# Optimization experiments

Measured on AMD Instinct MI355X. Metric: run time of the kernel, lower is better.

## Reference

```python
import math
import jax, jax.numpy as jnp
import numpy as np

# ---- static config (EquiformerV2 defaults; num_layers reduced to 2) ----
L_MAX, M_MAX = 6, 2
NC = (L_MAX + 1) ** 2          # 49 SH coefficients
C = 128                        # sphere_channels
H = 128                        # attn_hidden_channels
HEADS, VPH = 8, 16             # num_heads, attn_value_channels
FFN = 512                      # ffn_hidden_channels
NB = 600                       # gaussian distance basis count
NLAYERS = 2
N, E, G = 2048, 12288, 16      # nodes, edges, graphs
AVG_DEG = 3.0                  # edge-degree rescale factor (_AVG_DEGREE)
CUTOFF = 5.0
DISC_LO, DISC_HI = -3.26267, 3.295396

_deg = np.array([l for l in range(L_MAX + 1) for m in range(-l, l + 1)])
_mv = np.array([m for l in range(L_MAX + 1) for m in range(-l, l + 1)])
RESTRICT = np.nonzero(np.abs(_mv) <= M_MAX)[0]       # 29 coeffs with |m|<=mmax
NR = len(RESTRICT)
DEG1H = np.eye(L_MAX + 1, dtype=np.float32)[_deg]    # [49,7]
DEG_CNT = DEG1H.sum(0)                               # 2l+1 per degree

_off = np.linspace(0.0, CUTOFF, NB).astype(np.float32)
_gcoef = np.float32(-0.5 / (2.0 * (_off[1] - _off[0])) ** 2)  # width scalar 2.0

def gaussian_smearing(d):
    return jnp.exp(_gcoef * (d[:, None] - jnp.asarray(_off)[None, :]) ** 2)

def real_sph_harm(vec):
    # real spherical harmonics Y_lm of edge directions, [E, 49], l-major, m=-l..l
    r = jnp.linalg.norm(vec, axis=-1, keepdims=True)
    u = vec / jnp.maximum(r, 1e-8)
    x, y, z = u[:, 0], u[:, 1], u[:, 2]
    ct = jnp.clip(z, -1.0, 1.0)
    st = jnp.sqrt(jnp.clip(1.0 - ct * ct, 1e-12, 1.0))
    phi = jnp.arctan2(y, x)
    P = {(0, 0): jnp.ones_like(ct)}
    for m in range(1, L_MAX + 1):
        P[(m, m)] = -(2 * m - 1) * st * P[(m - 1, m - 1)]
    for m in range(0, L_MAX):
        P[(m + 1, m)] = (2 * m + 1) * ct * P[(m, m)]
    for m in range(0, L_MAX + 1):
        for l in range(m + 2, L_MAX + 1):
            P[(l, m)] = ((2 * l - 1) * ct * P[(l - 1, m)] - (l + m - 1) * P[(l - 2, m)]) / (l - m)
    cols = []
    for l in range(L_MAX + 1):
        for m in range(-l, l + 1):
            am = abs(m)
            nrm = math.sqrt((2 * l + 1) / (4 * math.pi) * math.factorial(l - am) / math.factorial(l + am))
            if m == 0:
                cols.append(nrm * P[(l, 0)])
            elif m > 0:
                cols.append(math.sqrt(2.0) * nrm * P[(l, m)] * jnp.cos(m * phi))
            else:
                cols.append(math.sqrt(2.0) * nrm * P[(l, am)] * jnp.sin(am * phi))
    return jnp.stack(cols, axis=-1)

def rms_norm_sh(x, w, eps=1e-6):
    # per-degree RMS over (m, channels) with learned [7,C] scale
    d1h = jnp.asarray(DEG1H)
    ms = jnp.einsum('nkc,kl->nl', x * x, d1h) / (jnp.asarray(DEG_CNT) * C)
    inv = 1.0 / jnp.sqrt(ms + eps)                      # [N,7]
    wk = jnp.einsum('lc,kl->kc', w, d1h)                # [49,C]
    return x * (inv @ d1h.T)[:, :, None] * wk[None]

def so2_attention(x, dist, src, dst, w_s, w_t, rw1, rb1, rw2, avec, w_v, w_p):
    n = x.shape[0]
    ridx = jnp.asarray(RESTRICT)
    xr = x[:, ridx, :]                                   # [N,29,C] (|m|<=mmax)
    msg = xr[src] @ w_s + xr[dst] @ w_t                  # [E,29,H]
    rad = jax.nn.silu(dist @ rw1 + rb1) @ rw2            # [E,H] radial modulation
    msg = msg * rad[:, None, :]
    a = jax.nn.silu(msg[:, 0, :]).reshape(-1, HEADS, H // HEADS)
    logits = jnp.einsum('ehd,hd->eh', a, avec)           # [E,HEADS]
    mx = jax.ops.segment_max(logits, dst, num_segments=n)
    ex = jnp.exp(logits - mx[dst])
    den = jax.ops.segment_sum(ex, dst, num_segments=n)
    alpha = ex / jnp.maximum(den[dst], 1e-9)
    v = (msg @ w_v).reshape(-1, NR, HEADS, VPH) * alpha[:, None, :, None]
    agg = jax.ops.segment_sum(v.reshape(-1, NR, HEADS * VPH), dst, num_segments=n)
    out_r = agg @ w_p                                    # [N,29,C]
    return jnp.zeros_like(x).at[:, ridx, :].set(out_r)

def ffn_act(x, w1, w2):
    # separable S2 activation: silu on l=0 scalars, sigmoid-gated higher degrees
    h = jnp.einsum('nkc,cf->nkf', x, w1)
    s = h[:, 0, :]
    h = jnp.concatenate([jax.nn.silu(s)[:, None, :], h[:, 1:, :] * jax.nn.sigmoid(s)[:, None, :]], axis=1)
    return jnp.einsum('nkf,fc->nkc', h, w2)

def _forward(pos, edge_vec, edge_index, batch, embed_table, deg_w1, deg_b1, deg_w2, deg_b2, deg_w3, attn_norm_w, w_src, w_tgt, rad_w1, rad_b1, rad_w2, alpha_vec, w_val, w_proj, ffn_norm_w, ffn_w1, ffn_w2, final_norm_w, lat_w_src, lat_w_tgt, lat_rad_w1, lat_rad_b1, lat_rad_w2, lat_alpha, lat_w_val, lat_w_proj):
    src, dst = edge_index[0], edge_index[1]
    d = jnp.linalg.norm(edge_vec, axis=-1)
    dist = gaussian_smearing(d)                                  # [E,600]
    # scalar node init from discretized coordinates (3 embedding lookups summed)
    t = jnp.clip(jnp.round((pos - DISC_LO) / (DISC_HI - DISC_LO) * 128.0 - 0.5), 0, 127).astype(jnp.int32)
    emb = embed_table[t[:, 0]] + embed_table[t[:, 1]] + embed_table[t[:, 2]]
    x = jnp.zeros((N, NC, C), emb.dtype).at[:, 0, :].set(emb)
    # edge-degree embedding: radial weights x Y_lm(edge dir), scatter to targets
    rad = jax.nn.silu(jax.nn.silu(dist @ deg_w1 + deg_b1) @ deg_w2 + deg_b2) @ deg_w3
    rad = rad.reshape(E, L_MAX + 1, C)[:, jnp.asarray(_deg), :]  # [E,49,C]
    Y = real_sph_harm(edge_vec)                                  # [E,49]
    x = x + jax.ops.segment_sum(Y[:, :, None] * rad, dst, num_segments=N) / AVG_DEG
    for i in range(NLAYERS):
        h = rms_norm_sh(x, attn_norm_w[i])
        x = x + so2_attention(h, dist, src, dst, w_src[i], w_tgt[i], rad_w1[i], rad_b1[i], rad_w2[i], alpha_vec[i], w_val[i], w_proj[i])
        h = rms_norm_sh(x, ffn_norm_w[i])
        x = x + ffn_act(h, ffn_w1[i], ffn_w2[i])
    x = rms_norm_sh(x, final_norm_w)
    latent = so2_attention(x, dist, src, dst, lat_w_src, lat_w_tgt, lat_rad_w1, lat_rad_b1, lat_rad_w2, lat_alpha, lat_w_val, lat_w_proj)
    cnt = jax.ops.segment_sum(jnp.ones((N,), latent.dtype), batch, num_segments=G)
    pooled = jax.ops.segment_sum(latent, batch, num_segments=G) / jnp.maximum(cnt, 1.0)[:, None, None]
    return pooled.reshape(1, -1)

def setup_inputs() -> dict:
    key = jax.random.key(0)
    ks = iter(jax.random.split(key, 64))
    def nrm(shape, fan_in):
        return jax.random.normal(next(ks), shape, jnp.float32) * np.float32(1.0 / math.sqrt(fan_in))
    inp = {}
    inp['pos'] = jax.random.normal(next(ks), (N, 3), jnp.float32) * 1.5
    inp['edge_vec'] = jax.random.normal(next(ks), (E, 3), jnp.float32)
    inp['edge_index'] = jax.random.randint(next(ks), (2, E), 0, N)
    inp['batch'] = jnp.sort(jax.random.randint(next(ks), (N,), 0, G))
    inp['embed_table'] = nrm((128, C), C)
    inp['deg_w1'] = nrm((NB, C), NB); inp['deg_b1'] = jnp.zeros((C,), jnp.float32)
    inp['deg_w2'] = nrm((C, C), C); inp['deg_b2'] = jnp.zeros((C,), jnp.float32)
    inp['deg_w3'] = nrm((C, (L_MAX + 1) * C), C)
    inp['attn_norm_w'] = jnp.ones((NLAYERS, L_MAX + 1, C), jnp.float32)
    inp['w_src'] = nrm((NLAYERS, C, H), C)
    inp['w_tgt'] = nrm((NLAYERS, C, H), C)
    inp['rad_w1'] = nrm((NLAYERS, NB, H), NB); inp['rad_b1'] = jnp.zeros((NLAYERS, H), jnp.float32)
    inp['rad_w2'] = nrm((NLAYERS, H, H), H)
    inp['alpha_vec'] = nrm((NLAYERS, HEADS, H // HEADS), H // HEADS)
    inp['w_val'] = nrm((NLAYERS, H, HEADS * VPH), H)
    inp['w_proj'] = nrm((NLAYERS, HEADS * VPH, C), HEADS * VPH)
    inp['ffn_norm_w'] = jnp.ones((NLAYERS, L_MAX + 1, C), jnp.float32)
    inp['ffn_w1'] = nrm((NLAYERS, C, FFN), C)
    inp['ffn_w2'] = nrm((NLAYERS, FFN, C), FFN)
    inp['final_norm_w'] = jnp.ones((L_MAX + 1, C), jnp.float32)
    inp['lat_w_src'] = nrm((C, H), C); inp['lat_w_tgt'] = nrm((C, H), C)
    inp['lat_rad_w1'] = nrm((NB, H), NB); inp['lat_rad_b1'] = jnp.zeros((H,), jnp.float32)
    inp['lat_rad_w2'] = nrm((H, H), H)
    inp['lat_alpha'] = nrm((HEADS, H // HEADS), H // HEADS)
    inp['lat_w_val'] = nrm((H, HEADS * VPH), H)
    inp['lat_w_proj'] = nrm((HEADS * VPH, C), HEADS * VPH)
    return inp

def reference(pos, edge_vec, edge_index, batch, embed_table, deg_w1, deg_b1, deg_w2, deg_b2, deg_w3, attn_norm_w, w_src, w_tgt, rad_w1, rad_b1, rad_w2, alpha_vec, w_val, w_proj, ffn_norm_w, ffn_w1, ffn_w2, final_norm_w, lat_w_src, lat_w_tgt, lat_rad_w1, lat_rad_b1, lat_rad_w2, lat_alpha, lat_w_val, lat_w_proj):
    return _forward(pos, edge_vec, edge_index, batch, embed_table, deg_w1, deg_b1, deg_w2, deg_b2, deg_w3, attn_norm_w, w_src, w_tgt, rad_w1, rad_b1, rad_w2, alpha_vec, w_val, w_proj, ffn_norm_w, ffn_w1, ffn_w2, final_norm_w, lat_w_src, lat_w_tgt, lat_rad_w1, lat_rad_b1, lat_rad_w2, lat_alpha, lat_w_val, lat_w_proj)
```

## Files before the change

kernel.cpp:

```cpp
#include <hip/hip_runtime.h>
#include <math.h>

#define NN 2048
#define NE 12288
#define NCO 49
#define NRr 29
#define CD 128
#define NG 16
#define NJOBS 21
#define VCH_E 6144

typedef unsigned short u16;
typedef short bhalf8 __attribute__((ext_vector_type(8)));
typedef float fvec4 __attribute__((ext_vector_type(4)));

__constant__ int c_res[29] = {0,1,2,3,4,5,6,7,8,10,11,12,13,14,18,19,20,21,22,28,29,30,31,32,40,41,42,43,44};
__constant__ int c_rinv[49] = {0,1,2,3,4,5,6,7,8,-1,9,10,11,12,13,-1,-1,-1,14,15,16,17,18,-1,-1,-1,-1,-1,19,20,21,22,23,-1,-1,-1,-1,-1,-1,-1,24,25,26,27,28,-1,-1,-1,-1};
__device__ constexpr int d_RES[29] = {0,1,2,3,4,5,6,7,8,10,11,12,13,14,18,19,20,21,22,28,29,30,31,32,40,41,42,43,44};

__device__ __forceinline__ constexpr int deg_of(int k){
  return (k<1)?0:(k<4)?1:(k<9)?2:(k<16)?3:(k<25)?4:(k<36)?5:6;
}
__device__ __forceinline__ float siluf(float x){ return x / (1.f + expf(-x)); }
__device__ __forceinline__ u16 f2bf(float f){
  unsigned int u = __float_as_uint(f);
  unsigned int r = (u + 0x7FFFu + ((u >> 16) & 1u)) >> 16;
  return (u16)r;
}
__device__ __forceinline__ float bf2f(u16 b){
  return __uint_as_float(((unsigned int)b) << 16);
}
__device__ __forceinline__ unsigned int pk(u16 lo, u16 hi){ return (unsigned int)lo | ((unsigned int)hi << 16); }

__global__ __launch_bounds__(1024) void k_hist4(const int* __restrict__ dst, int* __restrict__ cnt,
                                                int* __restrict__ CH){
  __shared__ int h[4*NN];
  for (int i = threadIdx.x; i < 4*NN; i += 1024) h[i] = 0;
  __syncthreads();
  const int QE = NE/4;
  for (int e = threadIdx.x; e < NE; e += 1024){
    int q = e / QE;
    atomicAdd(&h[q*NN + dst[e]], 1);
  }
  __syncthreads();
  for (int n = threadIdx.x; n < NN; n += 1024){
    int s = 0;
    #pragma unroll
    for (int q = 0; q < 4; q++){ int v = h[q*NN + n]; CH[q*NN + n] = v; s += v; }
    cnt[n] = s;
  }
}
__global__ __launch_bounds__(1024) void k_scan2(const int* __restrict__ cnt, int* __restrict__ rowptr){
  __shared__ int a[NN], b[NN];
  int t = threadIdx.x;
  for (int i = t; i < NN; i += 1024) a[i] = cnt[i];
  __syncthreads();
  int* pin = a; int* pout = b;
  for (int off = 1; off < NN; off <<= 1){
    for (int i = t; i < NN; i += 1024)
      pout[i] = pin[i] + ((i >= off) ? pin[i - off] : 0);
    __syncthreads();
    int* tmp = pin; pin = pout; pout = tmp;
  }
  for (int i = t; i < NN; i += 1024) rowptr[i + 1] = pin[i];
  if (t == 0) rowptr[0] = 0;
}
__global__ __launch_bounds__(256) void k_fillw4(const int* __restrict__ dst, const int* __restrict__ rowptr,
                                                const int* __restrict__ CH, int* __restrict__ eid){
  int q = threadIdx.x >> 6, lane = threadIdx.x & 63;
  int n = blockIdx.x;
  int base = rowptr[n];
  for (int qq = 0; qq < q; qq++) base += CH[qq*NN + n];
  const int QE = NE/4;
  for (int e0 = q*QE; e0 < (q+1)*QE; e0 += 64){
    int e = e0 + lane;
    bool m = (dst[e] == n);
    unsigned long long mask = __ballot(m);
    if (m) eid[base + __popcll(mask & ((1ull << lane) - 1ull))] = e;
    base += __popcll(mask);
  }
}
__global__ void k_gstart(const int* __restrict__ batch, int* __restrict__ gs){
  int g = threadIdx.x;
  if (g > NG) return;
  int lo = 0, hi = NN;
  while (lo < hi){ int mid = (lo + hi) >> 1; if (batch[mid] < g) lo = mid + 1; else hi = mid; }
  gs[g] = lo;
}

struct CastJobs {
  const float* src[NJOBS];
  u16* dst[NJOBS];
  int K[NJOBS], N[NJOBS];
  int start[NJOBS + 1];
  int total;
};
__global__ void k_castall(CastJobs J){
  int i = blockIdx.x*blockDim.x + threadIdx.x;
  if (i >= J.total) return;
  int j = 0;
  while (i >= J.start[j + 1]) j++;
  int local = i - J.start[j];
  int K = J.K[j], N = J.N[j];
  int n = local / K, k = local - n*K;
  J.dst[j][local] = f2bf(J.src[j][(size_t)k*N + n]);
}

__global__ void k_geom(const float* __restrict__ ev, float* __restrict__ Y, float* __restrict__ dv){
  int e = blockIdx.x*blockDim.x + threadIdx.x;
  if (e >= NE) return;
  float x = ev[e*3+0], y = ev[e*3+1], z = ev[e*3+2];
  float r = sqrtf(x*x + y*y + z*z);
  dv[e] = r;
  float rn = fmaxf(r, 1e-8f);
  float ux = x/rn, uy = y/rn, uz = z/rn;
  float ct = fminf(fmaxf(uz, -1.f), 1.f);
  float st = sqrtf(fminf(fmaxf(1.f - ct*ct, 1e-12f), 1.f));
  float phi = atan2f(uy, ux);
  float P[7][7];
  P[0][0] = 1.f;
  #pragma unroll
  for (int m = 1; m <= 6; m++) P[m][m] = -(2.f*m - 1.f)*st*P[m-1][m-1];
  #pragma unroll
  for (int m = 0; m <= 5; m++) P[m+1][m] = (2.f*m + 1.f)*ct*P[m][m];
  #pragma unroll
  for (int m = 0; m <= 6; m++){
    #pragma unroll
    for (int l = m+2; l <= 6; l++)
      P[l][m] = ((2.f*l - 1.f)*ct*P[l-1][m] - (float)(l+m-1)*P[l-2][m]) / (float)(l-m);
  }
  float cmv[7], smv[7];
  #pragma unroll
  for (int m = 0; m <= 6; m++){ cmv[m] = cosf((float)m*phi); smv[m] = sinf((float)m*phi); }
  const double FOURPI = 12.566370614359172;
  int k = 0;
  #pragma unroll
  for (int l = 0; l <= 6; l++){
    #pragma unroll
    for (int mm = -l; mm <= l; mm++){
      int am = mm < 0 ? -mm : mm;
      double ratio = 1.0;
      for (int i = l-am+1; i <= l+am; i++) ratio /= (double)i;
      double nrm = sqrt((2.0*l + 1.0)/FOURPI*ratio);
      float v;
      if (mm == 0)      v = (float)nrm * P[l][0];
      else if (mm > 0)  v = (float)(1.4142135623730951*nrm) * P[l][am] * cmv[am];
      else              v = (float)(1.4142135623730951*nrm) * P[l][am] * smv[am];
      Y[(size_t)e*49 + k] = v; k++;
    }
  }
}

__global__ __launch_bounds__(128) void k_rad1(const float* __restrict__ dv, const float* __restrict__ Wm,
                                              const float* __restrict__ bias, float* __restrict__ out){
  int e = blockIdx.x;
  int j = threadIdx.x;
  float d = dv[e];
  const float STEPF = (float)(5.0/599.0);
  const double step_d = (double)STEPF;
  const float GC = (float)(-0.5/((2.0*step_d)*(2.0*step_d)));
  __shared__ float g[64];
  int bc = (int)rintf(d / STEPF);
  int b0 = bc - 32;
  if (j < 64){
    int b = b0 + j;
    float gg = 0.f;
    if (b >= 0 && b < 600){
      float off = (float)((double)b * (5.0/599.0));
      float t = d - off;
      gg = expf(GC*t*t);
    }
    g[j] = gg;
  }
  __syncthreads();
  float acc = bias ? bias[j] : 0.f;
  #pragma unroll 8
  for (int i = 0; i < 64; i++){
    int b = b0 + i;
    if (b >= 0 && b < 600) acc += g[i]*Wm[b*CD + j];
  }
  out[(size_t)e*CD + j] = siluf(acc);
}

template<int AMODE, int EPI, int NT>
__global__ __launch_bounds__(256) void k_mgemm(
    const void* __restrict__ Av, const u16* __restrict__ Bt,
    const float* __restrict__ bias, void* __restrict__ Cv,
    int M, int N, int K, int lda,
    const float* __restrict__ P0,
    const int* __restrict__ src, const int* __restrict__ dstp,
    const int* __restrict__ eidp, const float* __restrict__ ALp, int e0)
{
  __shared__ __align__(16) u16 Asl[64*64];
  __shared__ __align__(16) u16 Bsl[NT][64*64];
  int tid = threadIdx.x;
  int bm = blockIdx.y*64;
  int bn0 = blockIdx.x*NT*64;
  int wid = tid >> 6, lane = tid & 63;
  int wr = wid >> 1, wc = wid & 1;
  int lr = lane & 15, lk = lane >> 4;
  fvec4 acc[NT][2][2] = {};
  for (int k0 = 0; k0 < K; k0 += 64){
    #pragma unroll
    for (int h = 0; h < 2; h++){
      int lin = tid + h*256;
      int row = lin >> 3, kg = lin & 7;
      uint4 q;
      if (AMODE == 3){
        int gr = bm + row;
        int el = gr / 29, kq = gr - el*29;
        int p = e0 + el;
        int e = eidp[p];
        int s = src[e], t = dstp[e];
        const u16* xst = (const u16*)P0;
        uint4 xs8 = *(const uint4*)&xst[((size_t)s*29 + kq)*256 + k0 + kg*8];
        uint4 xt8 = *(const uint4*)&xst[((size_t)t*29 + kq)*256 + 128 + k0 + kg*8];
        const float* rd = (const float*)Av + (size_t)e*128 + k0 + kg*8;
        const u16* xsp = (const u16*)&xs8;
        const u16* xtp = (const u16*)&xt8;
        u16 ov[8];
        #pragma unroll
        for (int j = 0; j < 8; j++)
          ov[j] = f2bf((bf2f(xsp[j]) + bf2f(xtp[j])) * rd[j]);
        q.x = pk(ov[0], ov[1]); q.y = pk(ov[2], ov[3]);
        q.z = pk(ov[4], ov[5]); q.w = pk(ov[6], ov[7]);
      } else if (AMODE == 2){
        const u16* ap = (const u16*)Av + (size_t)(bm + row)*lda + k0 + kg*8;
        q = *(const uint4*)ap;
      } else {
        const float* ap = (const float*)Av + (size_t)(bm + row)*lda + k0 + kg*8;
        float v[8];
        #pragma unroll
        for (int j = 0; j < 8; j++) v[j] = ap[j];
        q.x = pk(f2bf(v[0]), f2bf(v[1]));
        q.y = pk(f2bf(v[2]), f2bf(v[3]));
        q.z = pk(f2bf(v[4]), f2bf(v[5]));
        q.w = pk(f2bf(v[6]), f2bf(v[7]));
      }
      *(uint4*)&Asl[row*64 + ((kg*8) ^ ((row & 7)*8))] = q;
    }
    #pragma unroll
    for (int t = 0; t < NT; t++){
      #pragma unroll
      for (int h = 0; h < 2; h++){
        int lin = tid + h*256;
        int row = lin >> 3, kg = lin & 7;
        const u16* bp = Bt + (size_t)(bn0 + t*64 + row)*K + k0 + kg*8;
        *(uint4*)&Bsl[t][row*64 + ((kg*8) ^ ((row & 7)*8))] = *(const uint4*)bp;
      }
    }
    __syncthreads();
    #pragma unroll
    for (int ks = 0; ks < 2; ks++){
      int kg = ks*4 + lk;
      bhalf8 af[2];
      #pragma unroll
      for (int mi = 0; mi < 2; mi++){
        int ar = wr*32 + mi*16 + lr;
        af[mi] = *(const bhalf8*)&Asl[ar*64 + ((kg*8) ^ ((ar & 7)*8))];
      }
      #pragma unroll
      for (int t = 0; t < NT; t++){
        bhalf8 bfr[2];
        #pragma unroll
        for (int ni = 0; ni < 2; ni++){
          int br = wc*32 + ni*16 + lr;
          bfr[ni] = *(const bhalf8*)&Bsl[t][br*64 + ((kg*8) ^ ((br & 7)*8))];
        }
        #pragma unroll
        for (int mi = 0; mi < 2; mi++)
          #pragma unroll
          for (int ni = 0; ni < 2; ni++)
            acc[t][mi][ni] = __builtin_amdgcn_mfma_f32_16x16x32_bf16(af[mi], bfr[ni], acc[t][mi][ni], 0, 0, 0);
      }
    }
    __syncthreads();
  }
  #pragma unroll
  for (int t = 0; t < NT; t++){
    #pragma unroll
    for (int mi = 0; mi < 2; mi++){
      #pragma unroll
      for (int ni = 0; ni < 2; ni++){
        #pragma unroll
        for (int j = 0; j < 4; j++){
          int row = bm + wr*32 + mi*16 + lk*4 + j;
          int col = bn0 + t*64 + wc*32 + ni*16 + lr;
          float v = acc[t][mi][ni][j];
          if (EPI == 0){
            if (bias) v += bias[col];
            ((float*)Cv)[(size_t)row*N + col] = v;
          } else if (EPI == 1){
            if (bias) v += bias[col];
            ((float*)Cv)[(size_t)row*N + col] = siluf(v);
          } else if (EPI == 2){
            ((float*)Cv)[(size_t)row*N + col] += v;
          } else if (EPI == 3){
            int n = row / 29, kr = row - n*29;
            ((float*)Cv)[((size_t)n*49 + c_res[kr])*128 + col] += v;
          } else if (EPI == 4){
            ((float*)Cv)[(size_t)row*N + col] = 1.f/(1.f + expf(-v));
          } else if (EPI == 5){
            float g = P0[(size_t)(row/49)*N + col];
            ((u16*)Cv)[(size_t)row*N + col] = f2bf(v*g);
          } else if (EPI == 6){
            ((u16*)Cv)[(size_t)row*N + col] = f2bf(v);
          } else {
            int p = e0 + row/29;
            int e = eidp[p];
            float a = ALp[e*8 + (col >> 4)];
            ((u16*)Cv)[(size_t)row*N + col] = f2bf(v*a);
          }
        }
      }
    }
  }
}

__global__ __launch_bounds__(256) void k_aggseg(const u16* __restrict__ VS, const int* __restrict__ rowptr,
                                                int p0, int p1, int first, float* __restrict__ agg){
  int n = blockIdx.x;
  int a = rowptr[n], b = rowptr[n+1];
  if (a < p0) a = p0;
  if (b > p1) b = p1;
  int tid = threadIdx.x;
  for (int g = tid; g < 464; g += 256){
    size_t obase = (size_t)n*29*128 + (size_t)g*8;
    float s[8];
    if (first){
      #pragma unroll
      for (int j = 0; j < 8; j++) s[j] = 0.f;
    } else {
      float4 lo = *(const float4*)&agg[obase];
      float4 hi = *(const float4*)&agg[obase + 4];
      s[0]=lo.x; s[1]=lo.y; s[2]=lo.z; s[3]=lo.w;
      s[4]=hi.x; s[5]=hi.y; s[6]=hi.z; s[7]=hi.w;
    }
    for (int p = a; p < b; p++){
      uint4 q = *(const uint4*)&VS[(size_t)(p - p0)*3712 + (size_t)g*8];
      const u16* qp = (const u16*)&q;
      #pragma unroll
      for (int j = 0; j < 8; j++) s[j] += bf2f(qp[j]);
    }
    float4 lo, hi;
    lo.x=s[0]; lo.y=s[1]; lo.z=s[2]; lo.w=s[3];
    hi.x=s[4]; hi.y=s[5]; hi.z=s[6]; hi.w=s[7];
    *(float4*)&agg[obase] = lo;
    *(float4*)&agg[obase + 4] = hi;
  }
}

__global__ __launch_bounds__(128) void k_init(const float* __restrict__ pos, const float* __restrict__ table,
                                              const float* __restrict__ Yb, const float* __restrict__ radd,
                                              const int* __restrict__ rowptr, const int* __restrict__ eid,
                                              float* __restrict__ x){
  int n = blockIdx.x;
  int c = threadIdx.x;
  const float DLO = -3.26267f;
  const float DRG = (float)(3.295396 - (-3.26267));
  float p0 = pos[n*3+0], p1 = pos[n*3+1], p2 = pos[n*3+2];
  int t0 = min(127, max(0, (int)rintf((p0 - DLO)/DRG*128.f - 0.5f)));
  int t1 = min(127, max(0, (int)rintf((p1 - DLO)/DRG*128.f - 0.5f)));
  int t2 = min(127, max(0, (int)rintf((p2 - DLO)/DRG*128.f - 0.5f)));
  float emb = table[t0*CD + c] + table[t1*CD + c] + table[t2*CD + c];
  __shared__ float Yl[49];
  __shared__ float rl[896];
  float acc[NCO];
  #pragma unroll
  for (int k = 0; k < NCO; k++) acc[k] = 0.f;
  int pA = rowptr[n], pB = rowptr[n+1];
  for (int p = pA; p < pB; p++){
    int e = eid[p];
    if (c < 49) Yl[c] = Yb[(size_t)e*49 + c];
    #pragma unroll
    for (int q = 0; q < 7; q++) rl[q*128 + c] = radd[(size_t)e*896 + q*128 + c];
    __syncthreads();
    #pragma unroll
    for (int k = 0; k < NCO; k++){
      acc[k] += Yl[k]*rl[deg_of(k)*128 + c];
    }
    __syncthreads();
  }
  size_t base = (size_t)n*NCO*CD;
  x[base + c] = emb + acc[0]*(1.f/3.f);
  #pragma unroll
  for (int k = 1; k < NCO; k++) x[base + k*CD + c] = acc[k]*(1.f/3.f);
}

__global__ __launch_bounds__(128) void k_rmsnorm(const float* __restrict__ x, const float* __restrict__ w,
                                                 u16* __restrict__ out){
  int n = blockIdx.x;
  int c = threadIdx.x;
  const float* xb = x + (size_t)n*NCO*CD;
  float vals[NCO];
  float ss[7] = {0,0,0,0,0,0,0};
  #pragma unroll
  for (int k = 0; k < NCO; k++){
    float v = xb[k*CD + c];
    vals[k] = v;
    ss[deg_of(k)] += v*v;
  }
  __shared__ float red[7][128];
  #pragma unroll
  for (int l = 0; l < 7; l++) red[l][c] = ss[l];
  __syncthreads();
  __shared__ float inv[7];
  if (c < 7){
    float s = 0.f;
    for (int i = 0; i < 128; i++) s += red[c][i];
    float ms = s / ((float)(2*c + 1)*128.f);
    inv[c] = 1.f / sqrtf(ms + 1e-6f);
  }
  __syncthreads();
  size_t base = (size_t)n*NCO*CD;
  #pragma unroll
  for (int k = 0; k < NCO; k++){
    int l = deg_of(k);
    out[base + k*CD + c] = f2bf(vals[k]*inv[l]*w[l*CD + c]);
  }
}

__global__ __launch_bounds__(128) void k_rmsnormR(const float* __restrict__ x, const float* __restrict__ w,
                                                  u16* __restrict__ hr){
  int n = blockIdx.x;
  int c = threadIdx.x;
  const float* xb = x + (size_t)n*NCO*CD;
  float vals[NCO];
  float ss[7] = {0,0,0,0,0,0,0};
  #pragma unroll
  for (int k = 0; k < NCO; k++){
    float v = xb[k*CD + c];
    vals[k] = v;
    ss[deg_of(k)] += v*v;
  }
  __shared__ float red[7][128];
  #pragma unroll
  for (int l = 0; l < 7; l++) red[l][c] = ss[l];
  __syncthreads();
  __shared__ float inv[7];
  if (c < 7){
    float s = 0.f;
    for (int i = 0; i < 128; i++) s += red[c][i];
    float ms = s / ((float)(2*c + 1)*128.f);
    inv[c] = 1.f / sqrtf(ms + 1e-6f);
  }
  __syncthreads();
  size_t base = (size_t)n*NRr*CD;
  #pragma unroll
  for (int kr = 0; kr < NRr; kr++){
    int k = d_RES[kr];
    int l = deg_of(k);
    hr[base + kr*CD + c] = f2bf(vals[k]*inv[l]*w[l*CD + c]);
  }
}

__global__ __launch_bounds__(256) void k_attn(
    const u16* __restrict__ XST, const float* __restrict__ rad, const float* __restrict__ avec,
    const int* __restrict__ src, const int* __restrict__ rowptr, const int* __restrict__ eid,
    float* __restrict__ AL)
{
  int n = blockIdx.x;
  int p0 = rowptr[n], p1 = rowptr[n+1];
  int deg = p1 - p0;
  if (deg == 0) return;
  __shared__ float lgs[64][8];
  __shared__ float xt0[128];
  __shared__ float av[128];
  __shared__ float mxs[8], dens[8];
  int tid = threadIdx.x;
  if (tid < 128){
    xt0[tid] = bf2f(XST[(size_t)n*NRr*256 + 128 + tid]);
    av[tid] = avec[tid];
  }
  __syncthreads();
  for (int pair = tid; pair < deg*8; pair += 256){
    int pl = pair >> 3, h = pair & 7;
    int e = eid[p0 + pl];
    int s = src[e];
    const u16* xs = &XST[(size_t)s*NRr*256 + h*16];
    uint4 q0 = *(const uint4*)xs;
    uint4 q1 = *(const uint4*)(xs + 8);
    const u16* x0 = (const u16*)&q0;
    const u16* x1 = (const u16*)&q1;
    const float* rd = &rad[(size_t)e*128 + h*16];
    float4 r0 = *(const float4*)(rd + 0);
    float4 r1 = *(const float4*)(rd + 4);
    float4 r2 = *(const float4*)(rd + 8);
    float4 r3 = *(const float4*)(rd + 12);
    float rr[16] = {r0.x,r0.y,r0.z,r0.w, r1.x,r1.y,r1.z,r1.w,
                    r2.x,r2.y,r2.z,r2.w, r3.x,r3.y,r3.z,r3.w};
    float acc = 0.f;
    #pragma unroll
    for (int d = 0; d < 8; d++){
      float m = (bf2f(x0[d]) + xt0[h*16 + d]) * rr[d];
      acc += siluf(m) * av[h*16 + d];
    }
    #pragma unroll
    for (int d = 0; d < 8; d++){
      float m = (bf2f(x1[d]) + xt0[h*16 + 8 + d]) * rr[8 + d];
      acc += siluf(m) * av[h*16 + 8 + d];
    }
    lgs[pl][h] = acc;
  }
  __syncthreads();
  if (tid < 8){
    float m = -1e30f;
    for (int pl = 0; pl < deg; pl++) m = fmaxf(m, lgs[pl][tid]);
    float sden = 0.f;
    for (int pl = 0; pl < deg; pl++) sden += expf(lgs[pl][tid] - m);
    mxs[tid] = m; dens[tid] = sden;
  }
  __syncthreads();
  for (int pair = tid; pair < deg*8; pair += 256){
    int pl = pair >> 3, h = pair & 7;
    int e = eid[p0 + pl];
    AL[e*8 + h] = expf(lgs[pl][h] - mxs[h]) / fmaxf(dens[h], 1e-9f);
  }
}

__global__ void k_pool(const float* __restrict__ orr, const int* __restrict__ gs, float* __restrict__ out){
  int i = blockIdx.x*blockDim.x + threadIdx.x;
  if (i >= NG*NCO*CD) return;
  int c = i & 127;
  int k = (i >> 7) % 49;
  int g = i / (49*128);
  int kr = c_rinv[k];
  float v = 0.f;
  if (kr >= 0){
    int a = gs[g], b = gs[g+1];
    float s = 0.f;
    for (int n = a; n < b; n++) s += orr[((size_t)n*29 + kr)*128 + c];
    int cnt = b - a;
    v = s / (float)(cnt > 0 ? cnt : 1);
  }
  out[i] = v;
}

extern "C" void kernel_launch(void* const* d_in, const int* in_sizes, int n_in,
                              void* d_out, int out_size, void* d_ws, size_t ws_size,
                              hipStream_t stream){
  const float* pos    = (const float*)d_in[0];
  const float* evec   = (const float*)d_in[1];
  const int*   eidx   = (const int*)  d_in[2];
  const int*   batch  = (const int*)  d_in[3];
  const float* table  = (const float*)d_in[4];
  const float* deg_w1 = (const float*)d_in[5];
  const float* deg_b1 = (const float*)d_in[6];
  const float* deg_w2 = (const float*)d_in[7];
  const float* deg_b2 = (const float*)d_in[8];
  const float* deg_w3 = (const float*)d_in[9];
  const float* attn_nw= (const float*)d_in[10];
  const float* w_src  = (const float*)d_in[11];
  const float* w_tgt  = (const float*)d_in[12];
  const float* rad_w1 = (const float*)d_in[13];
  const float* rad_b1 = (const float*)d_in[14];
  const float* rad_w2 = (const float*)d_in[15];
  const float* avec   = (const float*)d_in[16];
  const float* w_val  = (const float*)d_in[17];
  const float* w_proj = (const float*)d_in[18];
  const float* ffn_nw = (const float*)d_in[19];
  const float* ffn_w1 = (const float*)d_in[20];
  const float* ffn_w2 = (const float*)d_in[21];
  const float* fin_nw = (const float*)d_in[22];
  const float* lw_src = (const float*)d_in[23];
  const float* lw_tgt = (const float*)d_in[24];
  const float* lrad_w1= (const float*)d_in[25];
  const float* lrad_b1= (const float*)d_in[26];
  const float* lrad_w2= (const float*)d_in[27];
  const float* lavec  = (const float*)d_in[28];
  const float* lw_val = (const float*)d_in[29];
  const float* lw_proj= (const float*)d_in[30];

  const int* srcp = eidx;
  const int* dstp = eidx + NE;

  float* W = (float*)d_ws;
  size_t o = 0;
  float* X    = W + o; o += (size_t)NN*49*128;
  float* Hb   = W + o; o += (size_t)NN*49*128;
  float* HR   = W + o; o += (size_t)NN*29*128;
  float* XSTf = W + o; o += (size_t)NN*29*256/2;
  float* R1   = W + o; o += (size_t)NE*128;
  float* R2   = W + o; o += (size_t)NE*128;
  float* Yb   = W + o; o += (size_t)NE*49;
  float* DV   = W + o; o += (size_t)NE;
  float* LG   = W + o; o += (size_t)NE*8;
  float* AL   = W + o; o += (size_t)NE*8;
  float* MX   = W + o; o += (size_t)NN*8;
  float* DEN  = W + o; o += (size_t)NN*8;
  float* SG   = W + o; o += (size_t)NN*512;
  int* CNT = (int*)(W + o); o += NN;
  int* RP  = (int*)(W + o); o += NN + 1;
  int* EID = (int*)(W + o); o += NE;
  int* GS  = (int*)(W + o); o += NG + 1;
  int* CH  = (int*)(W + o); o += 4*NN;
  u16* WB = (u16*)(W + o);
  size_t wo = 0;
  u16* T_degw2 = WB + wo; wo += 16384;
  u16* T_degw3 = WB + wo; wo += 114688;
  u16* T_wst[3]; u16* T_wv[3]; u16* T_wp[3]; u16* T_rw2[3];
  for (int i = 0; i < 3; i++){ T_wst[i] = WB + wo; wo += 32768; }
  for (int i = 0; i < 3; i++){ T_wv[i] = WB + wo; wo += 16384; }
  for (int i = 0; i < 3; i++){ T_wp[i] = WB + wo; wo += 16384; }
  for (int i = 0; i < 3; i++){ T_rw2[i] = WB + wo; wo += 16384; }
  u16* T_f1[2]; u16* T_f2[2];
  for (int i = 0; i < 2; i++){ T_f1[i] = WB + wo; wo += 65536; }
  for (int i = 0; i < 2; i++){ T_f2[i] = WB + wo; wo += 65536; }
  (void)ws_size; (void)in_sizes; (void)n_in; (void)out_size; (void)LG; (void)MX; (void)DEN;

  u16*  XSTw = (u16*)XSTf;
  u16*  HRw  = (u16*)HR;
  u16*  Hbw  = (u16*)Hb;
  float* RADD = Hb;
  u16*  VS    = (u16*)Hb;
  float* AG   = HR;
  float* OR_  = Hb;
  u16*  F1B   = (u16*)(Hb + (size_t)NN*49*64);

  {
    CastJobs J;
    int idx = 0, acc = 0;
    auto add = [&](const float* s, u16* d, int K, int N){
      J.src[idx] = s; J.dst[idx] = d; J.K[idx] = K; J.N[idx] = N; J.start[idx] = acc;
      acc += K*N; idx++;
    };
    add(deg_w2, T_degw2, 128, 128);
    add(deg_w3, T_degw3, 128, 896);
    for (int i = 0; i < 3; i++){
      add((i < 2) ? w_src  + (size_t)i*16384 : lw_src,  T_wst[i],          128, 128);
      add((i < 2) ? w_tgt  + (size_t)i*16384 : lw_tgt,  T_wst[i] + 16384,  128, 128);
      add((i < 2) ? w_val  + (size_t)i*16384 : lw_val,  T_wv[i], 128, 128);
      add((i < 2) ? w_proj + (size_t)i*16384 : lw_proj, T_wp[i], 128, 128);
      add((i < 2) ? rad_w2 + (size_t)i*16384 : lrad_w2, T_rw2[i], 128, 128);
    }
    for (int i = 0; i < 2; i++){
      add(ffn_w1 + (size_t)i*65536, T_f1[i], 128, 512);
      add(ffn_w2 + (size_t)i*65536, T_f2[i], 512, 128);
    }
    J.start[idx] = acc; J.total = acc;
    k_castall<<<(acc + 255)/256, 256, 0, stream>>>(J);
  }

  k_hist4<<<1, 1024, 0, stream>>>(dstp, CNT, CH);
  k_scan2<<<1, 1024, 0, stream>>>(CNT, RP);
  k_fillw4<<<NN, 256, 0, stream>>>(dstp, RP, CH, EID);
  k_gstart<<<1, 32, 0, stream>>>(batch, GS);

  k_geom<<<48, 256, 0, stream>>>(evec, Yb, DV);

  k_rad1<<<NE, 128, 0, stream>>>(DV, deg_w1, deg_b1, R1);
  k_mgemm<0,1,2><<<dim3(1, NE/64), 256, 0, stream>>>(R1, T_degw2, deg_b2, R2, NE, 128, 128, 128,
                                                     nullptr, nullptr, nullptr, nullptr, nullptr, 0);
  k_mgemm<0,0,2><<<dim3(7, NE/64), 256, 0, stream>>>(R2, T_degw3, nullptr, RADD, NE, 896, 128, 128,
                                                     nullptr, nullptr, nullptr, nullptr, nullptr, 0);
  k_init<<<NN, 128, 0, stream>>>(pos, table, Yb, RADD, RP, EID, X);

  for (int i = 0; i < 3; i++){
    const float* nw  = (i < 2) ? attn_nw + (size_t)i*896   : fin_nw;
    const float* rw1 = (i < 2) ? rad_w1 + (size_t)i*76800 : lrad_w1;
    const float* rb1 = (i < 2) ? rad_b1 + (size_t)i*128   : lrad_b1;
    const float* av  = (i < 2) ? avec   + (size_t)i*128   : lavec;

    k_rmsnormR<<<NN, 128, 0, stream>>>(X, nw, HRw);
    k_mgemm<2,6,4><<<dim3(1, NN*NRr/64), 256, 0, stream>>>(HRw, T_wst[i], nullptr, XSTw, NN*NRr, 256, 128, 128,
                                                           nullptr, nullptr, nullptr, nullptr, nullptr, 0);
    k_rad1<<<NE, 128, 0, stream>>>(DV, rw1, rb1, R1);
    k_mgemm<0,0,2><<<dim3(1, NE/64), 256, 0, stream>>>(R1, T_rw2[i], nullptr, R2, NE, 128, 128, 128,
                                                       nullptr, nullptr, nullptr, nullptr, nullptr, 0);
    k_attn<<<NN, 256, 0, stream>>>(XSTw, R2, av, srcp, RP, EID, AL);
    for (int ch = 0; ch < NE/VCH_E; ch++){
      int p0 = ch*VCH_E;
      k_mgemm<3,7,2><<<dim3(1, VCH_E*NRr/64), 256, 0, stream>>>(R2, T_wv[i], nullptr, VS,
                                                                VCH_E*NRr, 128, 128, 128,
                                                                (const float*)XSTw, srcp, dstp, EID, AL, p0);
      k_aggseg<<<NN, 256, 0, stream>>>(VS, RP, p0, p0 + VCH_E, ch == 0, AG);
    }
    if (i < 2){
      k_mgemm<0,3,2><<<dim3(1, NN*NRr/64), 256, 0, stream>>>(AG, T_wp[i], nullptr, X, NN*NRr, 128, 128, 128,
                                                             nullptr, nullptr, nullptr, nullptr, nullptr, 0);
      k_rmsnorm<<<NN, 128, 0, stream>>>(X, ffn_nw + (size_t)i*896, Hbw);
      k_mgemm<2,4,1><<<dim3(8, NN/64), 256, 0, stream>>>(Hbw, T_f1[i], nullptr, SG, NN, 512, 128, NCO*CD,
                                                         nullptr, nullptr, nullptr, nullptr, nullptr, 0);
      for (int half = 0; half < 2; half++){
        int n0 = half*(NN/2);
        int Mh = (NN/2)*NCO;
        k_mgemm<2,5,4><<<dim3(2, Mh/64), 256, 0, stream>>>(Hbw + (size_t)n0*NCO*CD, T_f1[i], nullptr, F1B,
                                                           Mh, 512, 128, 128,
                                                           SG + (size_t)n0*512, nullptr, nullptr, nullptr, nullptr, 0);
        k_mgemm<2,2,2><<<dim3(1, Mh/64), 256, 0, stream>>>(F1B, T_f2[i], nullptr, X + (size_t)n0*NCO*CD,
                                                           Mh, 128, 512, 512,
                                                           nullptr, nullptr, nullptr, nullptr, nullptr, 0);
      }
    } else {
      k_mgemm<0,0,2><<<dim3(1, NN*NRr/64), 256, 0, stream>>>(AG, T_wp[i], nullptr, OR_, NN*NRr, 128, 128, 128,
                                                             nullptr, nullptr, nullptr, nullptr, nullptr, 0);
      k_pool<<<(NG*NCO*CD + 255)/256, 256, 0, stream>>>(OR_, GS, (float*)d_out);
    }
  }
}
```

Measured before the change: 1.003 ms.

## Fuse FFN up-projection, gating and down-projection into one kernel

Replaces the two-pass FFN (a GEMM writing the gated 512-wide hidden activations to a bf16 buffer, then a second GEMM reading them back) with one kernel. Each block keeps a 64-row input tile in shared memory, loops over 64-wide hidden chunks, computes the gated hidden chunk into LDS and immediately accumulates the down-projection into registers, then adds the result into X. This removes the round trip of the ~100M-element intermediate through global memory and several launches. In exchange the W1/W2 chunks are reloaded by every block, there are three barriers per chunk, and the kernel uses about 56KB of LDS, which may limit occupancy.

```diff
diff --git a/kernel.cpp b/kernel.cpp
--- a/kernel.cpp
+++ b/kernel.cpp
@@ -317,6 +317,104 @@
   }
 }
 
+__global__ __launch_bounds__(256) void k_ffn(
+    const u16* __restrict__ A, const u16* __restrict__ W1, const u16* __restrict__ W2,
+    const float* __restrict__ SGp, float* __restrict__ Xp)
+{
+  __shared__ __align__(16) u16 Asl[64*128];
+  __shared__ __align__(16) u16 W1s[64*128];
+  __shared__ __align__(16) u16 W2s[128*64];
+  __shared__ __align__(16) u16 Hs[64*64];
+  int tid = threadIdx.x;
+  int bm = blockIdx.x*64;
+  int wid = tid >> 6, lane = tid & 63;
+  int wr = wid >> 1, wc = wid & 1;
+  int lr = lane & 15, lk = lane >> 4;
+  for (int g = tid; g < 1024; g += 256){
+    int row = g >> 4, kg = g & 15;
+    *(uint4*)&Asl[row*128 + ((kg*8) ^ ((row & 7)*16))] = *(const uint4*)&A[(size_t)(bm + row)*128 + kg*8];
+  }
+  fvec4 o[2][4] = {};
+  for (int h0 = 0; h0 < 512; h0 += 64){
+    for (int g = tid; g < 1024; g += 256){
+      int row = g >> 4, kg = g & 15;
+      *(uint4*)&W1s[row*128 + ((kg*8) ^ ((row & 7)*16))] = *(const uint4*)&W1[(size_t)(h0 + row)*128 + kg*8];
+    }
+    for (int g = tid; g < 1024; g += 256){
+      int row = g >> 3, kg = g & 7;
+      *(uint4*)&W2s[row*64 + ((kg*8) ^ ((row & 7)*8))] = *(const uint4*)&W2[(size_t)row*512 + h0 + kg*8];
+    }
+    __syncthreads();
+    fvec4 hid[2][2] = {};
+    #pragma unroll
+    for (int kk = 0; kk < 4; kk++){
+      int kg = kk*4 + lk;
+      bhalf8 af[2], bf[2];
+      #pragma unroll
+      for (int mi = 0; mi < 2; mi++){
+        int ar = wr*32 + mi*16 + lr;
+        af[mi] = *(const bhalf8*)&Asl[ar*128 + ((kg*8) ^ ((ar & 7)*16))];
+      }
+      #pragma unroll
+      for (int ni = 0; ni < 2; ni++){
+        int br = wc*32 + ni*16 + lr;
+        bf[ni] = *(const bhalf8*)&W1s[br*128 + ((kg*8) ^ ((br & 7)*16))];
+      }
+      #pragma unroll
+      for (int mi = 0; mi < 2; mi++)
+        #pragma unroll
+        for (int ni = 0; ni < 2; ni++)
+          hid[mi][ni] = __builtin_amdgcn_mfma_f32_16x16x32_bf16(af[mi], bf[ni], hid[mi][ni], 0, 0, 0);
+    }
+    #pragma unroll
+    for (int mi = 0; mi < 2; mi++){
+      #pragma unroll
+      for (int j = 0; j < 4; j++){
+        int row = wr*32 + mi*16 + lk*4 + j;
+        int node = (bm + row)/49;
+        const float* sgrow = &SGp[(size_t)node*512 + h0];
+        #pragma unroll
+        for (int ni = 0; ni < 2; ni++){
+          int col = wc*32 + ni*16 + lr;
+          Hs[row*64 + (col ^ ((row & 7)*8))] = f2bf(hid[mi][ni][j]*sgrow[col]);
+        }
+      }
+    }
+    __syncthreads();
+    #pragma unroll
+    for (int kk2 = 0; kk2 < 2; kk2++){
+      int kg = kk2*4 + lk;
+      bhalf8 af2[2], bf2[4];
+      #pragma unroll
+      for (int mi = 0; mi < 2; mi++){
+        int ar = wr*32 + mi*16 + lr;
+        af2[mi] = *(const bhalf8*)&Hs[ar*64 + ((kg*8) ^ ((ar & 7)*8))];
+      }
+      #pragma unroll
+      for (int ni = 0; ni < 4; ni++){
+        int br = wc*64 + ni*16 + lr;
+        bf2[ni] = *(const bhalf8*)&W2s[br*64 + ((kg*8) ^ ((br & 7)*8))];
+      }
+      #pragma unroll
+      for (int mi = 0; mi < 2; mi++)
+        #pragma unroll
+        for (int ni = 0; ni < 4; ni++)
+          o[mi][ni] = __builtin_amdgcn_mfma_f32_16x16x32_bf16(af2[mi], bf2[ni], o[mi][ni], 0, 0, 0);
+    }
+    __syncthreads();
+  }
+  #pragma unroll
+  for (int mi = 0; mi < 2; mi++)
+    #pragma unroll
+    for (int ni = 0; ni < 4; ni++)
+      #pragma unroll
+      for (int j = 0; j < 4; j++){
+        int row = bm + wr*32 + mi*16 + lk*4 + j;
+        int col = wc*64 + ni*16 + lr;
+        Xp[(size_t)row*128 + col] += o[mi][ni][j];
+      }
+}
+
 __global__ __launch_bounds__(256) void k_aggseg(const u16* __restrict__ VS, const int* __restrict__ rowptr,
                                                 int p0, int p1, int first, float* __restrict__ agg){
   int n = blockIdx.x;
@@ -615,7 +713,6 @@
   u16*  VS    = (u16*)Hb;
   float* AG   = HR;
   float* OR_  = Hb;
-  u16*  F1B   = (u16*)(Hb + (size_t)NN*49*64);
 
   {
     CastJobs J;
@@ -681,16 +778,7 @@
       k_rmsnorm<<<NN, 128, 0, stream>>>(X, ffn_nw + (size_t)i*896, Hbw);
       k_mgemm<2,4,1><<<dim3(8, NN/64), 256, 0, stream>>>(Hbw, T_f1[i], nullptr, SG, NN, 512, 128, NCO*CD,
                                                          nullptr, nullptr, nullptr, nullptr, nullptr, 0);
-      for (int half = 0; half < 2; half++){
-        int n0 = half*(NN/2);
-        int Mh = (NN/2)*NCO;
-        k_mgemm<2,5,4><<<dim3(2, Mh/64), 256, 0, stream>>>(Hbw + (size_t)n0*NCO*CD, T_f1[i], nullptr, F1B,
-                                                           Mh, 512, 128, 128,
-                                                           SG + (size_t)n0*512, nullptr, nullptr, nullptr, nullptr, 0);
-        k_mgemm<2,2,2><<<dim3(1, Mh/64), 256, 0, stream>>>(F1B, T_f2[i], nullptr, X + (size_t)n0*NCO*CD,
-                                                           Mh, 128, 512, 512,
-                                                           nullptr, nullptr, nullptr, nullptr, nullptr, 0);
-      }
+      k_ffn<<<NN*NCO/64, 256, 0, stream>>>(Hbw, T_f1[i], T_f2[i], SG, X);
     } else {
       k_mgemm<0,0,2><<<dim3(1, NN*NRr/64), 256, 0, stream>>>(AG, T_wp[i], nullptr, OR_, NN*NRr, 128, 128, 128,
                                                              nullptr, nullptr, nullptr, nullptr, nullptr, 0);
```

After: 982.6 us. 1.02x faster.
